# Performance work log

Measured on AMD Instinct MI355X. Metric: run time of the kernel, lower is better.

Reference implementation:

```python
import jax, jax.numpy as jnp
import numpy as np

D_MODEL = 2048
NUM_HEADS = 32
NUM_GROUPS = 8
HEAD_DIM = D_MODEL // NUM_HEADS  # 64
HPG = NUM_HEADS // NUM_GROUPS    # heads per group = 4
B, S = 2, 2048


def setup_inputs() -> dict:
    key = jax.random.key(0)
    ks = jax.random.split(key, 11)
    sd = 1.0 / np.sqrt(D_MODEL)
    kv_dim = HEAD_DIM * NUM_GROUPS
    return {
        "q": jax.random.normal(ks[0], (B, S, D_MODEL), jnp.float32),
        "k": jax.random.normal(ks[1], (B, S, D_MODEL), jnp.float32),
        "v": jax.random.normal(ks[2], (B, S, D_MODEL), jnp.float32),
        "Wq": jax.random.normal(ks[3], (D_MODEL, D_MODEL), jnp.float32) * sd,
        "bq": jnp.zeros((D_MODEL,), jnp.float32),
        "Wk": jax.random.normal(ks[4], (D_MODEL, kv_dim), jnp.float32) * sd,
        "bk": jnp.zeros((kv_dim,), jnp.float32),
        "Wv": jax.random.normal(ks[5], (D_MODEL, kv_dim), jnp.float32) * sd,
        "bv": jnp.zeros((kv_dim,), jnp.float32),
        "Wo": jax.random.normal(ks[6], (D_MODEL, D_MODEL), jnp.float32) * sd,
        "bo": jnp.zeros((D_MODEL,), jnp.float32),
    }


def reference(q, k, v, Wq, bq, Wk, bk, Wv, bv, Wo, bo):
    b, qlen, _ = q.shape
    kvlen = k.shape[1]
    # projections
    qh = (q @ Wq + bq).reshape(b, qlen, NUM_GROUPS, HPG, HEAD_DIM)   # [b,s,g,h,d]
    kh = (k @ Wk + bk).reshape(b, kvlen, NUM_GROUPS, HEAD_DIM)        # [b,t,g,d]
    vh = (v @ Wv + bv).reshape(b, kvlen, NUM_GROUPS, HEAD_DIM)        # [b,t,g,d]
    scale = 1.0 / np.sqrt(HEAD_DIM).astype(np.float32)
    # grouped attention: each group's heads share the same K/V
    scores = jnp.einsum('bsghd,btgd->bghst', qh, kh) * scale          # [b,g,h,s,t]
    attn = jax.nn.softmax(scores, axis=-1)                            # dropout = identity (eval)
    out = jnp.einsum('bghst,btgd->bsghd', attn, vh)                   # [b,s,g,h,d]
    out = out.reshape(b, qlen, D_MODEL)
    return out @ Wo + bo
```

## Files before the change

kernel.cpp:

```cpp
#include <hip/hip_runtime.h>

typedef unsigned short u16;
typedef unsigned int u32;
typedef __attribute__((ext_vector_type(8))) short bf16x8;
typedef __attribute__((ext_vector_type(4))) float f32x4;
typedef __attribute__((ext_vector_type(16))) float f32x16;

#define DM 2048
#define SQ_SCALE (0.125f * 1.44269504089f)

__device__ __forceinline__ u16 f2bf(float f) {
  union { float f; u32 u; } v; v.f = f;
  u32 r = v.u + 0x7fffu + ((v.u >> 16) & 1u);
  return (u16)(r >> 16);
}
__device__ __forceinline__ u32 pkrn(float lo, float hi) {
  union { float f; u32 u; } a, b; a.f = lo; b.f = hi;
  return ((a.u + 0x8000u) >> 16) | ((b.u + 0x8000u) & 0xffff0000u);
}
__device__ __forceinline__ u32 cvtpk(float lo, float hi) {
  u32 r;
  asm("v_cvt_pk_bf16_f32 %0, %1, %2" : "=v"(r) : "v"(lo), "v"(hi));
  return r;
}
__device__ __forceinline__ void gload16(const u16* g, u16* l) {
  __builtin_amdgcn_global_load_lds((const __attribute__((address_space(1))) void*)g,
                                   (__attribute__((address_space(3))) void*)l, 16, 0, 0);
}

__global__ __launch_bounds__(256) void cast3(const float* __restrict__ a0,
                                             const float* __restrict__ a1,
                                             const float* __restrict__ a2,
                                             u16* __restrict__ o0,
                                             u16* __restrict__ o1,
                                             u16* __restrict__ o2) {
  const float* in; u16* out;
  if (blockIdx.z == 0) { in = a0; out = o0; }
  else if (blockIdx.z == 1) { in = a1; out = o1; }
  else { in = a2; out = o2; }
  size_t i = ((size_t)blockIdx.x * 256 + threadIdx.x) * 8;
  float4 f0 = *(const float4*)(in + i);
  float4 f1 = *(const float4*)(in + i + 4);
  uint4 w = {pkrn(f0.x, f0.y), pkrn(f0.z, f0.w), pkrn(f1.x, f1.y), pkrn(f1.z, f1.w)};
  *(uint4*)(out + i) = w;
}

__global__ __launch_bounds__(256) void transpose_cast(const float* __restrict__ in,
                                                      u16* __restrict__ out,
                                                      int K, int N) {
  __shared__ u16 s[64][72];
  int n0 = blockIdx.x * 64, k0 = blockIdx.y * 64;
  int t = threadIdx.x;
  int r = t >> 2;
  int cc = (t & 3) * 16;
  const float* ip = in + (size_t)(k0 + r) * N + n0 + cc;
  u16 tmp[16];
#pragma unroll
  for (int i = 0; i < 16; i += 4) {
    float4 v = *(const float4*)(ip + i);
    tmp[i] = f2bf(v.x); tmp[i + 1] = f2bf(v.y);
    tmp[i + 2] = f2bf(v.z); tmp[i + 3] = f2bf(v.w);
  }
  *(uint4*)&s[r][cc] = *(uint4*)tmp;
  *(uint4*)&s[r][cc + 8] = *(uint4*)(tmp + 8);
  __syncthreads();
#pragma unroll
  for (int i = 0; i < 16; i++) tmp[i] = s[cc + i][r];
  u16* op = out + (size_t)(n0 + r) * K + k0 + cc;
  *(uint4*)op = *(uint4*)tmp;
  *(uint4*)(op + 8) = *(uint4*)(tmp + 8);
}

__global__ __launch_bounds__(256) void transpose_v(const u16* __restrict__ kvb,
                                                   u16* __restrict__ vtb) {
  __shared__ u16 s[64][72];
  int bg = blockIdx.y;
  int t0 = blockIdx.x * 64;
  int t = threadIdx.x;
  int r = t >> 2;
  int cc = (t & 3) * 16;
  const u16* ip = kvb + ((size_t)(bg >> 3) * 2048 + t0 + r) * 1024 + 512 + (bg & 7) * 64 + cc;
  *(uint4*)&s[r][cc] = *(const uint4*)ip;
  *(uint4*)&s[r][cc + 8] = *(const uint4*)(ip + 8);
  __syncthreads();
  u16 tmp[16];
#pragma unroll
  for (int i = 0; i < 16; i++) tmp[i] = s[cc + i][r];
  u16* op = vtb + (size_t)bg * 64 * 2048 + (size_t)r * 2048 + t0 + cc;
  *(uint4*)op = *(uint4*)tmp;
  *(uint4*)(op + 8) = *(uint4*)(tmp + 8);
}

__global__ __launch_bounds__(256) void gemm_proj(const u16* __restrict__ qb,
                                                 const u16* __restrict__ kb,
                                                 const u16* __restrict__ vb,
                                                 const u16* __restrict__ Bt,
                                                 const float* __restrict__ bqp,
                                                 const float* __restrict__ bkp,
                                                 const float* __restrict__ bvp,
                                                 u16* __restrict__ qhb,
                                                 u16* __restrict__ kvb) {
  __shared__ u16 As[128 * 32];
  __shared__ u16 Bs[128 * 32];
  int n0 = blockIdx.x * 128, m0 = blockIdx.y * 128;
  const u16* A; const float* bias; u16* C; int cw, bofs; float esc;
  if (n0 < 2048)      { A = qb; bias = bqp; C = qhb; cw = 2048; bofs = 0;    esc = SQ_SCALE; }
  else if (n0 < 2560) { A = kb; bias = bkp; C = kvb; cw = 1024; bofs = 2048; esc = 1.0f; }
  else                { A = vb; bias = bvp; C = kvb; cw = 1024; bofs = 2560; esc = 1.0f; }
  int ccol0 = (n0 < 2048) ? n0 : (n0 - 2048);

  int tid = threadIdx.x, wave = tid >> 6, lane = tid & 63;
  int lq = lane & 15, quad = lane >> 4;
  int wm = (wave & 1) * 64, wn = (wave >> 1) * 64;

  f32x4 zero = {0.f, 0.f, 0.f, 0.f};
  f32x4 acc[4][4];
#pragma unroll
  for (int i = 0; i < 4; i++)
#pragma unroll
    for (int j = 0; j < 4; j++) acc[i][j] = zero;

  const u16* gA = A + (size_t)(m0 + wave * 16 + (lane >> 2)) * 2048 + (lane & 3) * 8;
  const u16* gB = Bt + (size_t)(n0 + wave * 16 + (lane >> 2)) * 2048 + (lane & 3) * 8;
  u16* lA0 = &As[(wave * 16) * 32];
  u16* lA1 = &As[(64 + wave * 16) * 32];
  u16* lB0 = &Bs[(wave * 16) * 32];
  u16* lB1 = &Bs[(64 + wave * 16) * 32];

  for (int k0 = 0; k0 < 2048; k0 += 32) {
    __syncthreads();
    gload16(gA + k0, lA0);
    gload16(gA + (size_t)64 * 2048 + k0, lA1);
    gload16(gB + k0, lB0);
    gload16(gB + (size_t)64 * 2048 + k0, lB1);
    __syncthreads();
    bf16x8 af[4], bf[4];
#pragma unroll
    for (int i = 0; i < 4; i++) af[i] = *(const bf16x8*)&As[(wm + i * 16 + lq) * 32 + quad * 8];
#pragma unroll
    for (int j = 0; j < 4; j++) bf[j] = *(const bf16x8*)&Bs[(wn + j * 16 + lq) * 32 + quad * 8];
#pragma unroll
    for (int i = 0; i < 4; i++)
#pragma unroll
      for (int j = 0; j < 4; j++)
        acc[i][j] = __builtin_amdgcn_mfma_f32_16x16x32_bf16(af[i], bf[j], acc[i][j], 0, 0, 0);
  }
#pragma unroll
  for (int j = 0; j < 4; j++) {
    int nglob = n0 + wn + j * 16 + lq;
    float bv = bias[nglob - bofs];
    int col = ccol0 + wn + j * 16 + lq;
#pragma unroll
    for (int i = 0; i < 4; i++) {
#pragma unroll
      for (int rg = 0; rg < 4; rg++) {
        int row = m0 + wm + i * 16 + quad * 4 + rg;
        C[(size_t)row * cw + col] = f2bf((acc[i][j][rg] + bv) * esc);
      }
    }
  }
}

__global__ __launch_bounds__(256) void gemm_o(const u16* __restrict__ A,
                                              const u16* __restrict__ Bt,
                                              const float* __restrict__ bias,
                                              float* __restrict__ C) {
  __shared__ u16 As[128 * 32];
  __shared__ u16 Bs[128 * 32];
  int n0 = blockIdx.x * 128, m0 = blockIdx.y * 128;
  int tid = threadIdx.x, wave = tid >> 6, lane = tid & 63;
  int lq = lane & 15, quad = lane >> 4;
  int wm = (wave & 1) * 64, wn = (wave >> 1) * 64;

  f32x4 zero = {0.f, 0.f, 0.f, 0.f};
  f32x4 acc[4][4];
#pragma unroll
  for (int i = 0; i < 4; i++)
#pragma unroll
    for (int j = 0; j < 4; j++) acc[i][j] = zero;

  const u16* gA = A + (size_t)(m0 + wave * 16 + (lane >> 2)) * 2048 + (lane & 3) * 8;
  const u16* gB = Bt + (size_t)(n0 + wave * 16 + (lane >> 2)) * 2048 + (lane & 3) * 8;
  u16* lA0 = &As[(wave * 16) * 32];
  u16* lA1 = &As[(64 + wave * 16) * 32];
  u16* lB0 = &Bs[(wave * 16) * 32];
  u16* lB1 = &Bs[(64 + wave * 16) * 32];

  for (int k0 = 0; k0 < 2048; k0 += 32) {
    __syncthreads();
    gload16(gA + k0, lA0);
    gload16(gA + (size_t)64 * 2048 + k0, lA1);
    gload16(gB + k0, lB0);
    gload16(gB + (size_t)64 * 2048 + k0, lB1);
    __syncthreads();
    bf16x8 af[4], bf[4];
#pragma unroll
    for (int i = 0; i < 4; i++) af[i] = *(const bf16x8*)&As[(wm + i * 16 + lq) * 32 + quad * 8];
#pragma unroll
    for (int j = 0; j < 4; j++) bf[j] = *(const bf16x8*)&Bs[(wn + j * 16 + lq) * 32 + quad * 8];
#pragma unroll
    for (int i = 0; i < 4; i++)
#pragma unroll
      for (int j = 0; j < 4; j++)
        acc[i][j] = __builtin_amdgcn_mfma_f32_16x16x32_bf16(af[i], bf[j], acc[i][j], 0, 0, 0);
  }
#pragma unroll
  for (int j = 0; j < 4; j++) {
    int col = n0 + wn + j * 16 + lq;
    float bv = bias[col];
#pragma unroll
    for (int i = 0; i < 4; i++) {
#pragma unroll
      for (int rg = 0; rg < 4; rg++) {
        int row = m0 + wm + i * 16 + quad * 4 + rg;
        C[(size_t)row * 2048 + col] = acc[i][j][rg] + bv;
      }
    }
  }
}

__global__ __launch_bounds__(256) void attn2(const u16* __restrict__ qh,
                                             const u16* __restrict__ kvb,
                                             const u16* __restrict__ vtb,
                                             u16* __restrict__ out) {
  __shared__ u16 Ks[32][72];
  __shared__ u16 Vs[64][40];
  __shared__ float Ls[4][32];
  int flat = blockIdx.x + (blockIdx.y << 4);
  int w = ((flat & 7) << 7) + (flat >> 3);
  int head = w >> 4;
  int b = head >> 5, g = (head >> 2) & 7, h = head & 3;
  int tid = threadIdx.x, wave = tid >> 6, lane = tid & 63;
  int lh = lane & 31, hi = lane >> 5;
  const int qoff = (g * 4 + h) * 64;
  const int koff = g * 64;
  int sBase = (w & 15) * 128 + wave * 32;

  bf16x8 qf[4];
#pragma unroll
  for (int st = 0; st < 4; st++)
    qf[st] = *(const bf16x8*)(qh + (size_t)(b * 2048 + sBase + lh) * DM +
                              qoff + st * 16 + hi * 8);

  f32x16 o_acc[2];
#pragma unroll
  for (int db = 0; db < 2; db++)
#pragma unroll
    for (int r = 0; r < 16; r++) o_acc[db][r] = 0.f;
  float l_acc = 0.f;

  int sr = tid >> 3, sc = (tid & 7) * 8;
  int vd = tid >> 2, vc = (tid & 3) * 8;
  const u16* kbase = kvb + (size_t)b * 2048 * 1024 + koff;
  const u16* vbase = vtb + (size_t)(head >> 2) * 64 * 2048 + (size_t)vd * 2048;

  uint4 kreg = *(const uint4*)(kbase + (size_t)sr * 1024 + sc);
  uint4 vreg = *(const uint4*)(vbase + vc);

  for (int t0 = 0; t0 < 2048; t0 += 32) {
    __syncthreads();
    *(uint4*)&Ks[sr][sc] = kreg;
    *(uint4*)&Vs[vd][vc] = vreg;
    __syncthreads();
    int tn = (t0 + 32 < 2048) ? t0 + 32 : 0;
    kreg = *(const uint4*)(kbase + (size_t)(tn + sr) * 1024 + sc);
    vreg = *(const uint4*)(vbase + tn + vc);

    bf16x8 kf[4], vf[2][2];
#pragma unroll
    for (int st = 0; st < 4; st++) kf[st] = *(const bf16x8*)&Ks[lh][st * 16 + hi * 8];
#pragma unroll
    for (int T = 0; T < 2; T++)
#pragma unroll
      for (int db = 0; db < 2; db++)
        vf[T][db] = *(const bf16x8*)&Vs[db * 32 + lh][T * 16 + hi * 8];

    f32x16 st_acc;
#pragma unroll
    for (int r = 0; r < 16; r++) st_acc[r] = 0.f;
    __builtin_amdgcn_s_setprio(1);
#pragma unroll
    for (int st = 0; st < 4; st++)
      st_acc = __builtin_amdgcn_mfma_f32_32x32x16_bf16(kf[st], qf[st], st_acc, 0, 0, 0);
    __builtin_amdgcn_s_setprio(0);
    float pr[16];
#pragma unroll
    for (int r = 0; r < 16; r++) pr[r] = __builtin_amdgcn_exp2f(st_acc[r]);
    float s0 = ((pr[0] + pr[1]) + (pr[2] + pr[3])) + ((pr[4] + pr[5]) + (pr[6] + pr[7]));
    float s1 = ((pr[8] + pr[9]) + (pr[10] + pr[11])) + ((pr[12] + pr[13]) + (pr[14] + pr[15]));
    l_acc += s0 + s1;
    u32 pk[8];
#pragma unroll
    for (int a = 0; a < 4; a++) {
      pk[2 * a] = cvtpk(pr[4 * a], pr[4 * a + 1]);
      pk[2 * a + 1] = cvtpk(pr[4 * a + 2], pr[4 * a + 3]);
    }
#pragma unroll
    for (int T = 0; T < 2; T++) {
      u32 E0 = hi ? pk[4 * T] : pk[4 * T + 2];
      u32 E1 = hi ? pk[4 * T + 1] : pk[4 * T + 3];
      u32 X0 = __shfl_xor(E0, 32);
      u32 X1 = __shfl_xor(E1, 32);
      union { u32 u[4]; bf16x8 v; } af;
      af.u[0] = hi ? X0 : pk[4 * T];
      af.u[1] = hi ? X1 : pk[4 * T + 1];
      af.u[2] = hi ? pk[4 * T + 2] : X0;
      af.u[3] = hi ? pk[4 * T + 3] : X1;
      __builtin_amdgcn_s_setprio(1);
#pragma unroll
      for (int db = 0; db < 2; db++)
        o_acc[db] = __builtin_amdgcn_mfma_f32_32x32x16_bf16(af.v, vf[T][db], o_acc[db], 0, 0, 0);
      __builtin_amdgcn_s_setprio(0);
    }
  }

  {
    float lt = l_acc + __shfl_xor(l_acc, 32);
    Ls[wave][lh] = 1.0f / lt;
  }
  __builtin_amdgcn_wave_barrier();
  {
    f32x4 inv[4];
#pragma unroll
    for (int a = 0; a < 4; a++) inv[a] = *(const f32x4*)&Ls[wave][8 * a + 4 * hi];
#pragma unroll
    for (int db = 0; db < 2; db++) {
#pragma unroll
      for (int r = 0; r < 16; r++) {
        int srow = (r & 3) + 8 * (r >> 2) + 4 * hi;
        size_t o = (size_t)(b * 2048 + sBase + srow) * DM + qoff + db * 32 + lh;
        out[o] = f2bf(o_acc[db][r] * inv[r >> 2][r & 3]);
      }
    }
  }
}

extern "C" void kernel_launch(void* const* d_in, const int* in_sizes, int n_in,
                              void* d_out, int out_size, void* d_ws, size_t ws_size,
                              hipStream_t stream) {
  const float* q  = (const float*)d_in[0];
  const float* k  = (const float*)d_in[1];
  const float* v  = (const float*)d_in[2];
  const float* Wq = (const float*)d_in[3];
  const float* bq = (const float*)d_in[4];
  const float* Wk = (const float*)d_in[5];
  const float* bk = (const float*)d_in[6];
  const float* Wv = (const float*)d_in[7];
  const float* bv = (const float*)d_in[8];
  const float* Wo = (const float*)d_in[9];
  const float* bo = (const float*)d_in[10];

  u16* p = (u16*)d_ws;
  u16* WqkvT = p; p += (size_t)3072 * 2048;
  u16* WoT   = p; p += (size_t)2048 * 2048;
  u16* qb    = p; p += (size_t)4096 * 2048;
  u16* kb    = p; p += (size_t)4096 * 2048;
  u16* vb    = p; p += (size_t)4096 * 2048;
  u16* qhb   = p; p += (size_t)4096 * 2048;
  u16* kvb   = p; p += (size_t)4096 * 1024;
  u16* vtb   = p; p += (size_t)16 * 64 * 2048;
  u16* att   = qb;

  cast3<<<dim3(4096, 1, 3), 256, 0, stream>>>(q, k, v, qb, kb, vb);

  transpose_cast<<<dim3(32, 32), 256, 0, stream>>>(Wq, WqkvT, 2048, 2048);
  transpose_cast<<<dim3(8, 32), 256, 0, stream>>>(Wk, WqkvT + (size_t)2048 * 2048, 2048, 512);
  transpose_cast<<<dim3(8, 32), 256, 0, stream>>>(Wv, WqkvT + (size_t)2560 * 2048, 2048, 512);
  transpose_cast<<<dim3(32, 32), 256, 0, stream>>>(Wo, WoT, 2048, 2048);

  gemm_proj<<<dim3(24, 32), 256, 0, stream>>>(qb, kb, vb, WqkvT, bq, bk, bv, qhb, kvb);

  transpose_v<<<dim3(32, 16), 256, 0, stream>>>(kvb, vtb);

  attn2<<<dim3(16, 64), 256, 0, stream>>>(qhb, kvb, vtb, att);

  gemm_o<<<dim3(16, 32), 256, 0, stream>>>(att, WoT, bo, (float*)d_out);
}
```

Baseline: 411.5 us.

## Split attention KV range across two wave halves and merge partial outputs

The attention block grows to 512 threads: two groups of four waves each handle half of the key/value sequence for the same 128 query rows, each with its own shared K/V staging buffers. At the end the second half writes its partial output and row-sum into shared memory (a union reusing the staging space), and the first half adds them in before normalising and storing. The aim is more waves in flight per block and half the serial loop length per wave, to hide load and MFMA latency. The cost is an extra shared-memory reduction with two block barriers, a larger shared footprint, and register pressure under the 512-thread launch bound. The merge relies on the kernel's unshifted exp2 softmax, so no running maximum has to be reconciled.

```diff
diff --git a/kernel.cpp b/kernel.cpp
--- a/kernel.cpp
+++ b/kernel.cpp
@@ -219,22 +219,24 @@
   }
 }
 
-__global__ __launch_bounds__(256) void attn2(const u16* __restrict__ qh,
-                                             const u16* __restrict__ kvb,
-                                             const u16* __restrict__ vtb,
-                                             u16* __restrict__ out) {
-  __shared__ u16 Ks[32][72];
-  __shared__ u16 Vs[64][40];
-  __shared__ float Ls[4][32];
+__global__ __launch_bounds__(512, 8) void attn2(const u16* __restrict__ qh,
+                                                const u16* __restrict__ kvb,
+                                                const u16* __restrict__ vtb,
+                                                u16* __restrict__ out) {
+  __shared__ union {
+    struct { u16 Ks[2][32][72]; u16 Vs[2][64][40]; } s;
+    struct { float Ox[4][32][64]; float Lx[4][32]; float Ls[4][32]; } e;
+  } sm;
   int flat = blockIdx.x + (blockIdx.y << 4);
   int w = ((flat & 7) << 7) + (flat >> 3);
   int head = w >> 4;
   int b = head >> 5, g = (head >> 2) & 7, h = head & 3;
   int tid = threadIdx.x, wave = tid >> 6, lane = tid & 63;
+  int thalf = wave >> 2, swave = wave & 3;
   int lh = lane & 31, hi = lane >> 5;
   const int qoff = (g * 4 + h) * 64;
   const int koff = g * 64;
-  int sBase = (w & 15) * 128 + wave * 32;
+  int sBase = (w & 15) * 128 + swave * 32;
 
   bf16x8 qf[4];
 #pragma unroll
@@ -249,31 +251,32 @@
     for (int r = 0; r < 16; r++) o_acc[db][r] = 0.f;
   float l_acc = 0.f;
 
-  int sr = tid >> 3, sc = (tid & 7) * 8;
-  int vd = tid >> 2, vc = (tid & 3) * 8;
-  const u16* kbase = kvb + (size_t)b * 2048 * 1024 + koff;
-  const u16* vbase = vtb + (size_t)(head >> 2) * 64 * 2048 + (size_t)vd * 2048;
+  int htid = tid & 255;
+  int sr = htid >> 3, sc = (htid & 7) * 8;
+  int vd = htid >> 2, vc = (htid & 3) * 8;
+  const u16* kbase = kvb + (size_t)b * 2048 * 1024 + koff + (size_t)thalf * 1024 * 1024;
+  const u16* vbase = vtb + (size_t)(head >> 2) * 64 * 2048 + (size_t)vd * 2048 + thalf * 1024;
 
   uint4 kreg = *(const uint4*)(kbase + (size_t)sr * 1024 + sc);
   uint4 vreg = *(const uint4*)(vbase + vc);
 
-  for (int t0 = 0; t0 < 2048; t0 += 32) {
-    __syncthreads();
-    *(uint4*)&Ks[sr][sc] = kreg;
-    *(uint4*)&Vs[vd][vc] = vreg;
-    __syncthreads();
-    int tn = (t0 + 32 < 2048) ? t0 + 32 : 0;
+  for (int t0 = 0; t0 < 1024; t0 += 32) {
+    __syncthreads();
+    *(uint4*)&sm.s.Ks[thalf][sr][sc] = kreg;
+    *(uint4*)&sm.s.Vs[thalf][vd][vc] = vreg;
+    __syncthreads();
+    int tn = (t0 + 32 < 1024) ? t0 + 32 : 0;
     kreg = *(const uint4*)(kbase + (size_t)(tn + sr) * 1024 + sc);
     vreg = *(const uint4*)(vbase + tn + vc);
 
     bf16x8 kf[4], vf[2][2];
 #pragma unroll
-    for (int st = 0; st < 4; st++) kf[st] = *(const bf16x8*)&Ks[lh][st * 16 + hi * 8];
+    for (int st = 0; st < 4; st++) kf[st] = *(const bf16x8*)&sm.s.Ks[thalf][lh][st * 16 + hi * 8];
 #pragma unroll
     for (int T = 0; T < 2; T++)
 #pragma unroll
       for (int db = 0; db < 2; db++)
-        vf[T][db] = *(const bf16x8*)&Vs[db * 32 + lh][T * 16 + hi * 8];
+        vf[T][db] = *(const bf16x8*)&sm.s.Vs[thalf][db * 32 + lh][T * 16 + hi * 8];
 
     f32x16 st_acc;
 #pragma unroll
@@ -314,15 +317,33 @@
     }
   }
 
-  {
-    float lt = l_acc + __shfl_xor(l_acc, 32);
-    Ls[wave][lh] = 1.0f / lt;
-  }
-  __builtin_amdgcn_wave_barrier();
-  {
+  float lt = l_acc + __shfl_xor(l_acc, 32);
+  __syncthreads();
+  if (thalf == 1) {
+#pragma unroll
+    for (int db = 0; db < 2; db++)
+#pragma unroll
+      for (int r = 0; r < 16; r++) {
+        int srow = (r & 3) + 8 * (r >> 2) + 4 * hi;
+        sm.e.Ox[swave][srow][db * 32 + lh] = o_acc[db][r];
+      }
+    if (hi == 0) sm.e.Lx[swave][lh] = lt;
+  }
+  __syncthreads();
+  if (thalf == 0) {
+    lt += sm.e.Lx[swave][lh];
+#pragma unroll
+    for (int db = 0; db < 2; db++)
+#pragma unroll
+      for (int r = 0; r < 16; r++) {
+        int srow = (r & 3) + 8 * (r >> 2) + 4 * hi;
+        o_acc[db][r] += sm.e.Ox[swave][srow][db * 32 + lh];
+      }
+    sm.e.Ls[swave][lh] = 1.0f / lt;
+    __builtin_amdgcn_wave_barrier();
     f32x4 inv[4];
 #pragma unroll
-    for (int a = 0; a < 4; a++) inv[a] = *(const f32x4*)&Ls[wave][8 * a + 4 * hi];
+    for (int a = 0; a < 4; a++) inv[a] = *(const f32x4*)&sm.e.Ls[swave][8 * a + 4 * hi];
 #pragma unroll
     for (int db = 0; db < 2; db++) {
 #pragma unroll
@@ -372,7 +393,7 @@
 
   transpose_v<<<dim3(32, 16), 256, 0, stream>>>(kvb, vtb);
 
-  attn2<<<dim3(16, 64), 256, 0, stream>>>(qhb, kvb, vtb, att);
+  attn2<<<dim3(16, 64), 512, 0, stream>>>(qhb, kvb, vtb, att);
 
   gemm_o<<<dim3(16, 32), 256, 0, stream>>>(att, WoT, bo, (float*)d_out);
 }
```

After: 1.338 ms. +225.0%, slower.

## Write transposed V from projection epilogue and double-buffer attention LDS tiles

Applied to the files above, without the earlier changes.

The V projection epilogue now writes its output directly in transposed [b,g,d,t] layout, so the separate transpose_v kernel and its extra pass through memory are removed. The attention kernel's K/V shared-memory tiles become double-buffered, cutting the per-iteration barriers from two to one. In exchange the transposed stores from the GEMM epilogue are 8-byte writes strided across rows, which coalesce less well. The single barrier relies on the alternating buffers to avoid overwriting a tile that is still being read.

```diff
diff --git a/kernel.cpp b/kernel.cpp
--- a/kernel.cpp
+++ b/kernel.cpp
@@ -71,26 +71,6 @@
   *(uint4*)(op + 8) = *(uint4*)(tmp + 8);
 }
 
-__global__ __launch_bounds__(256) void transpose_v(const u16* __restrict__ kvb,
-                                                   u16* __restrict__ vtb) {
-  __shared__ u16 s[64][72];
-  int bg = blockIdx.y;
-  int t0 = blockIdx.x * 64;
-  int t = threadIdx.x;
-  int r = t >> 2;
-  int cc = (t & 3) * 16;
-  const u16* ip = kvb + ((size_t)(bg >> 3) * 2048 + t0 + r) * 1024 + 512 + (bg & 7) * 64 + cc;
-  *(uint4*)&s[r][cc] = *(const uint4*)ip;
-  *(uint4*)&s[r][cc + 8] = *(const uint4*)(ip + 8);
-  __syncthreads();
-  u16 tmp[16];
-#pragma unroll
-  for (int i = 0; i < 16; i++) tmp[i] = s[cc + i][r];
-  u16* op = vtb + (size_t)bg * 64 * 2048 + (size_t)r * 2048 + t0 + cc;
-  *(uint4*)op = *(uint4*)tmp;
-  *(uint4*)(op + 8) = *(uint4*)(tmp + 8);
-}
-
 __global__ __launch_bounds__(256) void gemm_proj(const u16* __restrict__ qb,
                                                  const u16* __restrict__ kb,
                                                  const u16* __restrict__ vb,
@@ -99,7 +79,8 @@
                                                  const float* __restrict__ bkp,
                                                  const float* __restrict__ bvp,
                                                  u16* __restrict__ qhb,
-                                                 u16* __restrict__ kvb) {
+                                                 u16* __restrict__ kvb,
+                                                 u16* __restrict__ vtb) {
   __shared__ u16 As[128 * 32];
   __shared__ u16 Bs[128 * 32];
   int n0 = blockIdx.x * 128, m0 = blockIdx.y * 128;
@@ -145,17 +126,35 @@
       for (int j = 0; j < 4; j++)
         acc[i][j] = __builtin_amdgcn_mfma_f32_16x16x32_bf16(af[i], bf[j], acc[i][j], 0, 0, 0);
   }
-#pragma unroll
-  for (int j = 0; j < 4; j++) {
-    int nglob = n0 + wn + j * 16 + lq;
-    float bv = bias[nglob - bofs];
-    int col = ccol0 + wn + j * 16 + lq;
-#pragma unroll
-    for (int i = 0; i < 4; i++) {
-#pragma unroll
-      for (int rg = 0; rg < 4; rg++) {
-        int row = m0 + wm + i * 16 + quad * 4 + rg;
-        C[(size_t)row * cw + col] = f2bf((acc[i][j][rg] + bv) * esc);
+  if (n0 >= 2560) {
+#pragma unroll
+    for (int j = 0; j < 4; j++) {
+      int cv = (n0 - 2560) + wn + j * 16 + lq;
+      float bvv = bias[cv];
+      u16* vout = vtb + (size_t)cv * 2048;
+#pragma unroll
+      for (int i = 0; i < 4; i++) {
+        int row = m0 + wm + i * 16 + quad * 4;
+        int bb = row >> 11, tt = row & 2047;
+        u16 w4[4];
+#pragma unroll
+        for (int rg = 0; rg < 4; rg++) w4[rg] = f2bf(acc[i][j][rg] + bvv);
+        *(uint2*)(vout + (size_t)bb * 8 * 64 * 2048 + tt) = *(uint2*)w4;
+      }
+    }
+  } else {
+#pragma unroll
+    for (int j = 0; j < 4; j++) {
+      int nglob = n0 + wn + j * 16 + lq;
+      float bv = bias[nglob - bofs];
+      int col = ccol0 + wn + j * 16 + lq;
+#pragma unroll
+      for (int i = 0; i < 4; i++) {
+#pragma unroll
+        for (int rg = 0; rg < 4; rg++) {
+          int row = m0 + wm + i * 16 + quad * 4 + rg;
+          C[(size_t)row * cw + col] = f2bf((acc[i][j][rg] + bv) * esc);
+        }
       }
     }
   }
@@ -223,8 +222,8 @@
                                              const u16* __restrict__ kvb,
                                              const u16* __restrict__ vtb,
                                              u16* __restrict__ out) {
-  __shared__ u16 Ks[32][72];
-  __shared__ u16 Vs[64][40];
+  __shared__ u16 Ks[2][32][72];
+  __shared__ u16 Vs[2][64][40];
   __shared__ float Ls[4][32];
   int flat = blockIdx.x + (blockIdx.y << 4);
   int w = ((flat & 7) << 7) + (flat >> 3);
@@ -257,23 +256,23 @@
   uint4 kreg = *(const uint4*)(kbase + (size_t)sr * 1024 + sc);
   uint4 vreg = *(const uint4*)(vbase + vc);
 
+  int c = 0;
   for (int t0 = 0; t0 < 2048; t0 += 32) {
-    __syncthreads();
-    *(uint4*)&Ks[sr][sc] = kreg;
-    *(uint4*)&Vs[vd][vc] = vreg;
-    __syncthreads();
+    *(uint4*)&Ks[c][sr][sc] = kreg;
+    *(uint4*)&Vs[c][vd][vc] = vreg;
     int tn = (t0 + 32 < 2048) ? t0 + 32 : 0;
     kreg = *(const uint4*)(kbase + (size_t)(tn + sr) * 1024 + sc);
     vreg = *(const uint4*)(vbase + tn + vc);
+    __syncthreads();
 
     bf16x8 kf[4], vf[2][2];
 #pragma unroll
-    for (int st = 0; st < 4; st++) kf[st] = *(const bf16x8*)&Ks[lh][st * 16 + hi * 8];
+    for (int st = 0; st < 4; st++) kf[st] = *(const bf16x8*)&Ks[c][lh][st * 16 + hi * 8];
 #pragma unroll
     for (int T = 0; T < 2; T++)
 #pragma unroll
       for (int db = 0; db < 2; db++)
-        vf[T][db] = *(const bf16x8*)&Vs[db * 32 + lh][T * 16 + hi * 8];
+        vf[T][db] = *(const bf16x8*)&Vs[c][db * 32 + lh][T * 16 + hi * 8];
 
     f32x16 st_acc;
 #pragma unroll
@@ -312,6 +311,7 @@
         o_acc[db] = __builtin_amdgcn_mfma_f32_32x32x16_bf16(af.v, vf[T][db], o_acc[db], 0, 0, 0);
       __builtin_amdgcn_s_setprio(0);
     }
+    c ^= 1;
   }
 
   {
@@ -368,9 +368,7 @@
   transpose_cast<<<dim3(8, 32), 256, 0, stream>>>(Wv, WqkvT + (size_t)2560 * 2048, 2048, 512);
   transpose_cast<<<dim3(32, 32), 256, 0, stream>>>(Wo, WoT, 2048, 2048);
 
-  gemm_proj<<<dim3(24, 32), 256, 0, stream>>>(qb, kb, vb, WqkvT, bq, bk, bv, qhb, kvb);
-
-  transpose_v<<<dim3(32, 16), 256, 0, stream>>>(kvb, vtb);
+  gemm_proj<<<dim3(24, 32), 256, 0, stream>>>(qb, kb, vb, WqkvT, bq, bk, bv, qhb, kvb, vtb);
 
   attn2<<<dim3(16, 64), 256, 0, stream>>>(qhb, kvb, vtb, att);
 
```

After: 430.6 us. +4.6%, slower.
